# Kernel tuning notes

Hardware: AMD Instinct MI355X
Metric: run time of the kernel (lower is better)

The kernel has to match this reference:

```python
import jax, jax.numpy as jnp
import numpy as np

NR, K = 175, 250              # num_ranges, top_k
N = NR * K                    # 43750 active radar points
SHAPE0 = (56, 350, 512)       # (ele, range, azi) full-res sparse grid
SHAPE1 = (28, 175, 256)       # after stride-2 sparse conv
SHAPE2 = (14, 88, 128)        # after second stride-2 sparse conv
CAP1 = 350000                 # <= 8*N unique active cells after stride-2 conv
CAP2 = 69000                  # reachable region bound at stage 2 (14*88*56)
BC = 16                       # base_channel
C1, C2, CO = 2 * BC, 8 * BC, 128
OFFS = [(a, b, c) for a in range(3) for b in range(3) for c in range(3)]


def bn(x, p):
    # BatchNorm1d (eval form): p = [gamma, beta, running_mean, running_var]
    g, b, m, v = p
    return (x - m) * jax.lax.rsqrt(v + 1e-3) * g + b


def gn(x, groups, gamma, beta):
    n, c = x.shape
    xr = x.reshape(n, groups, c // groups)
    m = xr.mean(-1, keepdims=True)
    v = ((xr - m) ** 2).mean(-1, keepdims=True)
    return ((xr - m) * jax.lax.rsqrt(v + 1e-5)).reshape(n, c) * gamma + beta


def build_lut(coords, shape, n):
    # dense coord -> row-index map; out-of-bounds (padded) coords are dropped
    lut = jnp.full(shape, -1, jnp.int32)
    return lut.at[coords[:, 0], coords[:, 1], coords[:, 2]].set(jnp.arange(n, dtype=jnp.int32), mode='drop')


def subm_conv(feats, coords, lut, shape, w):
    # submanifold 3x3x3 conv: outputs only at active sites (gather-GEMM-accumulate)
    S = jnp.array(shape, jnp.int32)
    out = jnp.zeros((feats.shape[0], w.shape[-1]), feats.dtype)
    for k, off in enumerate(OFFS):
        nb = coords + (jnp.array(off, jnp.int32) - 1)
        inb = jnp.all((nb >= 0) & (nb < S), axis=-1)
        nbc = jnp.clip(nb, 0, S - 1)
        idx = lut[nbc[:, 0], nbc[:, 1], nbc[:, 2]]
        ok = inb & (idx >= 0)
        f = jnp.where(ok[:, None], feats[jnp.maximum(idx, 0)], 0.0)
        out = out + f @ w[k]
    return out


def down_conv(feats, coords_in, lut_in, shape_in, shape_out, cap, w):
    # SparseConv3d k=3 stride=2 pad=1: output sites = cells with any active input in receptive field
    mask = jnp.zeros(shape_in, bool).at[coords_in[:, 0], coords_in[:, 1], coords_in[:, 2]].set(True, mode='drop')
    pm = jnp.pad(mask, 1)
    om = jnp.zeros(shape_out, bool)
    for (a, b, c) in OFFS:
        om = om | pm[a:a + 2 * shape_out[0]:2, b:b + 2 * shape_out[1]:2, c:c + 2 * shape_out[2]:2]
    i0, i1, i2 = jnp.nonzero(om, size=cap, fill_value=0)
    oc = jnp.stack([i0, i1, i2], -1).astype(jnp.int32)
    valid = jnp.arange(cap) < om.sum()
    S = jnp.array(shape_in, jnp.int32)
    out = jnp.zeros((cap, w.shape[-1]), feats.dtype)
    for k, off in enumerate(OFFS):
        nb = 2 * oc + (jnp.array(off, jnp.int32) - 1)   # input coord = 2j + k - 1
        inb = jnp.all((nb >= 0) & (nb < S), axis=-1)
        nbc = jnp.clip(nb, 0, S - 1)
        idx = lut_in[nbc[:, 0], nbc[:, 1], nbc[:, 2]]
        ok = inb & (idx >= 0)
        f = jnp.where(ok[:, None], feats[jnp.maximum(idx, 0)], 0.0)
        out = out + f @ w[k]
    # padded (invalid) rows get out-of-bounds coords so later scatters/luts drop them
    oc_safe = jnp.where(valid[:, None], oc, jnp.array(shape_out, jnp.int32))
    return out, oc_safe


def basic_block(f, coords, lut, shape, w2, p2):
    h = jax.nn.relu(bn(subm_conv(f, coords, lut, shape, w2[0]), p2[0]))
    h = bn(subm_conv(h, coords, lut, shape, w2[1]), p2[1])
    return jax.nn.relu(h + f)


def range_attn(pw, c1, c3, ele_table, azi_table, wq, bq, wk, bk, wv, bv):
    x = pw.reshape(NR, K, 1)
    e = ele_table[c1.reshape(NR, K)]   # [NR,K,3]
    a = azi_table[c3.reshape(NR, K)]   # [NR,K,3]
    scale = 32.0 ** -0.5               # queries.size(-1) = hidden_dim = 32
    for l in range(4):
        xin = jnp.concatenate([x, e, a], -1)           # [NR,K,7]
        q = xin @ wq[l] + bq[l]
        kk = xin @ wk[l] + bk[l]
        v = xin @ wv[l] + bv[l]
        att = jax.nn.softmax(jnp.einsum('rkd,rjd->rkj', q, kk) * scale, axis=-1)
        x = jnp.einsum('rkj,rjd->rkd', att, v)         # [NR,K,1]
    return x.reshape(N, 1)


def forward(voxel_features, coors, ele_table, azi_table, wq, bq, wk, bk, wv, bv,
            w_in, b_in, gin_g, gin_b, w_d1, bn_d1, w_r1, bn_r1,
            w_d2, bn_d2, w_r2, bn_r2, w_out, b_out, gout_g, gout_b):
    c1, c2, c3 = coors[:, 1], coors[:, 2], coors[:, 3]
    pw = jnp.log10(voxel_features[:, -2])[:, None]
    f_att = range_attn(pw, c1, c3, ele_table, azi_table, wq, bq, wk, bk, wv, bv)
    ele = c1 * 2 - 9          # (56 - 37*2)//2 = -9
    rng = c2 * 2
    azi = c3 * 2 + 149        # (512 - 107*2)//2 = 149
    feats = jnp.concatenate([ele[:, None].astype(jnp.float32), rng[:, None].astype(jnp.float32),
                             azi[:, None].astype(jnp.float32), f_att], -1)   # [N,4]
    coords0 = jnp.stack([ele, rng, azi], -1).astype(jnp.int32)
    # conv_input: 1x1x1 SubMConv (per-point linear) + GroupNorm(8) + ReLU
    f0 = jax.nn.relu(gn(feats @ w_in + b_in, 8, gin_g, gin_b))
    lut0 = build_lut(coords0, SHAPE0, N)
    f1, oc1 = down_conv(f0, coords0, lut0, SHAPE0, SHAPE1, CAP1, w_d1)
    f1 = jax.nn.relu(bn(f1, bn_d1))
    lut1 = build_lut(oc1, SHAPE1, CAP1)
    f1 = basic_block(f1, oc1, lut1, SHAPE1, w_r1[0], bn_r1[0])
    f1 = basic_block(f1, oc1, lut1, SHAPE1, w_r1[1], bn_r1[1])
    f2, oc2 = down_conv(f1, oc1, lut1, SHAPE1, SHAPE2, CAP2, w_d2)
    f2 = jax.nn.relu(bn(f2, bn_d2))
    lut2 = build_lut(oc2, SHAPE2, CAP2)
    f2 = basic_block(f2, oc2, lut2, SHAPE2, w_r2[0], bn_r2[0])
    f2 = basic_block(f2, oc2, lut2, SHAPE2, w_r2[1], bn_r2[1])
    # conv_out: SubMConv3d(k=3, bias) + GroupNorm(16) + ReLU
    fo = subm_conv(f2, oc2, lut2, SHAPE2, w_out) + b_out
    fo = jax.nn.relu(gn(fo, 16, gout_g, gout_b))
    dense = jnp.zeros(SHAPE2 + (CO,), fo.dtype).at[oc2[:, 0], oc2[:, 1], oc2[:, 2]].set(fo, mode='drop')
    # torch dense: [1,C,ele,range,azi].permute(0,1,4,3,2) -> [1,C,azi,range,ele]
    return jnp.transpose(dense, (3, 2, 1, 0))[None]


def setup_inputs():
    key = jax.random.key(0)
    ks = iter(jax.random.split(key, 64))
    nrm = lambda shp, s: jax.random.normal(next(ks), shp, jnp.float32) * s

    def bnp(c):
        return jnp.stack([1.0 + nrm((c,), 0.1), nrm((c,), 0.1), nrm((c,), 0.05),
                          1.0 + 0.1 * jax.random.uniform(next(ks), (c,), jnp.float32)])

    voxel_features = jax.random.uniform(next(ks), (N, 2), jnp.float32, 0.1, 100.0)
    c0 = jnp.zeros((N,), jnp.int32)
    c1 = jax.random.randint(next(ks), (N,), 5, 33, jnp.int32)      # ele bin -> ele_ind in [1,55]
    c2 = jnp.repeat(jnp.arange(NR, dtype=jnp.int32), K)            # 250 points per range bin
    c3 = jax.random.randint(next(ks), (N,), 0, 107, jnp.int32)
    coors = jnp.stack([c0, c1, c2, c3], -1)
    return dict(
        voxel_features=voxel_features, coors=coors, batch_size=1,
        ele_table=nrm((37, 3), 1.0), azi_table=nrm((107, 3), 1.0),
        wq=nrm((4, 7, 32), 0.3), bq=nrm((4, 32), 0.1),
        wk=nrm((4, 7, 32), 0.3), bk=nrm((4, 32), 0.1),
        wv=nrm((4, 7, 1), 0.3), bv=nrm((4, 1), 0.1),
        w_in=nrm((4, BC), 0.5), b_in=nrm((BC,), 0.1),
        gin_g=1.0 + nrm((BC,), 0.1), gin_b=nrm((BC,), 0.1),
        w_d1=nrm((27, BC, C1), (27 * BC) ** -0.5), bn_d1=bnp(C1),
        w_r1=nrm((2, 2, 27, C1, C1), (27 * C1) ** -0.5),
        bn_r1=jnp.stack([jnp.stack([bnp(C1), bnp(C1)]), jnp.stack([bnp(C1), bnp(C1)])]),
        w_d2=nrm((27, C1, C2), (27 * C1) ** -0.5), bn_d2=bnp(C2),
        w_r2=nrm((2, 2, 27, C2, C2), (27 * C2) ** -0.5),
        bn_r2=jnp.stack([jnp.stack([bnp(C2), bnp(C2)]), jnp.stack([bnp(C2), bnp(C2)])]),
        w_out=nrm((27, C2, CO), (27 * C2) ** -0.5), b_out=nrm((CO,), 0.1),
        gout_g=1.0 + nrm((CO,), 0.1), gout_b=nrm((CO,), 0.1),
    )


def reference(voxel_features, coors, batch_size, ele_table, azi_table, wq, bq, wk, bk, wv, bv,
              w_in, b_in, gin_g, gin_b, w_d1, bn_d1, w_r1, bn_r1,
              w_d2, bn_d2, w_r2, bn_r2, w_out, b_out, gout_g, gout_b):
    assert batch_size == 1
    return forward(voxel_features, coors, ele_table, azi_table, wq, bq, wk, bk, wv, bv,
                   w_in, b_in, gin_g, gin_b, w_d1, bn_d1, w_r1, bn_r1,
                   w_d2, bn_d2, w_r2, bn_r2, w_out, b_out, gout_g, gout_b)
```

## Files before the change

kernel.cpp:

```cpp
#include <hip/hip_runtime.h>
#include <math.h>

#define NRR 175
#define KK 250
#define NN (NRR*KK)

#define S0_0 56
#define S0_1 350
#define S0_2 512
#define S1_0 28
#define S1_1 175
#define S1_2 256
#define S2_0 14
#define S2_1 88
#define S2_2 128
#define CAP1 350000
#define CAP2 69000
#define C1 32
#define C2 128
#define FOP 69632

#define CELLS0 (S0_0*S0_1*S0_2)
#define CELLS1 (S1_0*S1_1*S1_2)
#define CELLS2 (S2_0*S2_1*S2_2)

#define ATT_SCALE 0.17677669529663687f

typedef __attribute__((ext_vector_type(8))) __bf16 bf16x8;
typedef __attribute__((ext_vector_type(16))) float f32x16;

__device__ __forceinline__ unsigned short f2b(float x) {
    unsigned int u = __builtin_bit_cast(unsigned int, x);
    unsigned int r = u + 0x7FFFu + ((u >> 16) & 1u);
    return (unsigned short)(r >> 16);
}
__device__ __forceinline__ float b2f(unsigned short h) {
    return __builtin_bit_cast(float, (unsigned int)h << 16);
}

__device__ __forceinline__ int block_incl_scan(int v, int* s) {
    int t = threadIdx.x;
    s[t] = v; __syncthreads();
    #pragma unroll
    for (int d = 1; d < 256; d <<= 1) {
        int x = (t >= d) ? s[t - d] : 0;
        __syncthreads();
        s[t] += x;
        __syncthreads();
    }
    return s[t];
}

__device__ __forceinline__ void cand(int p, int So, int* o, int& no) {
    no = 0;
    if ((p & 1) == 0) {
        int q = p >> 1; if (q < So) o[no++] = q;
    } else {
        int q = (p - 1) >> 1; if (q < So) o[no++] = q;
        q = (p + 1) >> 1;     if (q < So) o[no++] = q;
    }
}

__global__ __launch_bounds__(256) void k_init(const float* __restrict__ vf,
                                              const int* __restrict__ coors,
                                              float* __restrict__ x,
                                              int* __restrict__ lut0,
                                              int* __restrict__ om1) {
    int i = blockIdx.x * 256 + threadIdx.x;
    if (i >= NN) return;
    x[i] = log10f(vf[i * 2]);
    int c1 = coors[i * 4 + 1], c2 = coors[i * 4 + 2], c3 = coors[i * 4 + 3];
    int e = 2 * c1 - 9, rg = 2 * c2, az = 2 * c3 + 149;
    atomicMax(&lut0[(e * S0_1 + rg) * S0_2 + az], i);
    int A[2], B[2], C[2]; int na, nb, nc;
    cand(e, S1_0, A, na); cand(rg, S1_1, B, nb); cand(az, S1_2, C, nc);
    for (int ia = 0; ia < na; ia++)
        for (int ib = 0; ib < nb; ib++)
            for (int ic = 0; ic < nc; ic++)
                om1[(A[ia] * S1_1 + B[ib]) * S1_2 + C[ic]] = 1;
}

#define QS 40
__global__ __launch_bounds__(256, 1) void k_attn(float* __restrict__ x_io,
    const int* __restrict__ coors,
    const float* __restrict__ et, const float* __restrict__ at,
    const float* __restrict__ wq, const float* __restrict__ bq,
    const float* __restrict__ wk, const float* __restrict__ bk,
    const float* __restrict__ wv, const float* __restrict__ bv) {
    __shared__ float xin[KK * 7];
    __shared__ unsigned short ksh_h[256 * QS];
    __shared__ unsigned short ksh_l[256 * QS];
    __shared__ float vsh[256];
    const int r = blockIdx.x;
    const int t = threadIdx.x;
    const int w = t >> 6, ln = t & 63, l31 = ln & 31, lh = ln >> 5;

    for (int i = t; i < KK; i += 256) {
        int gi = r * KK + i;
        xin[i * 7 + 0] = x_io[gi];
        int c1 = coors[gi * 4 + 1], c3 = coors[gi * 4 + 3];
        xin[i * 7 + 1] = et[c1 * 3 + 0]; xin[i * 7 + 2] = et[c1 * 3 + 1]; xin[i * 7 + 3] = et[c1 * 3 + 2];
        xin[i * 7 + 4] = at[c3 * 3 + 0]; xin[i * 7 + 5] = at[c3 * 3 + 1]; xin[i * 7 + 6] = at[c3 * 3 + 2];
    }
    __syncthreads();

    union U8 { bf16x8 v; unsigned short u[8]; };

    for (int l = 0; l < 4; l++) {
        const float* wql = wq + l * 7 * 32; const float* bql = bq + l * 32;
        const float* wkl = wk + l * 7 * 32; const float* bkl = bk + l * 32;
        const float* wvl = wv + l * 7;      const float  bvl = bv[l];
        float qh_f[32], ql_f[32];
        if (t < KK) {
            float xi[7];
            #pragma unroll
            for (int ci = 0; ci < 7; ci++) xi[ci] = xin[t * 7 + ci];
            float av = bvl;
            #pragma unroll
            for (int ci = 0; ci < 7; ci++) av += xi[ci] * wvl[ci];
            vsh[t] = av;
            #pragma unroll
            for (int d = 0; d < 32; d++) {
                float aq = bql[d], ak = bkl[d];
                #pragma unroll
                for (int ci = 0; ci < 7; ci++) { aq += xi[ci] * wql[ci * 32 + d]; ak += xi[ci] * wkl[ci * 32 + d]; }
                aq *= ATT_SCALE;
                float h = b2f(f2b(aq));
                qh_f[d] = h; ql_f[d] = aq - h;
                unsigned short k16 = f2b(ak);
                ksh_h[t * QS + d] = k16;
                ksh_l[t * QS + d] = f2b(ak - b2f(k16));
            }
        } else {
            #pragma unroll
            for (int d = 0; d < 32; d++) {
                qh_f[d] = 0.f; ql_f[d] = 0.f;
                ksh_h[t * QS + d] = 0; ksh_l[t * QS + d] = 0;
            }
            vsh[t] = 0.f;
        }
        __syncthreads();

        U8 Bh[2][2], Bl[2][2];
        #pragma unroll
        for (int b = 0; b < 2; b++) {
            int src = b * 32 + l31;
            #pragma unroll
            for (int ks = 0; ks < 2; ks++) {
                #pragma unroll
                for (int j = 0; j < 8; j++) {
                    float h0 = __shfl(qh_f[ks * 16 + j],     src, 64);
                    float h1 = __shfl(qh_f[ks * 16 + 8 + j], src, 64);
                    float l0 = __shfl(ql_f[ks * 16 + j],     src, 64);
                    float l1 = __shfl(ql_f[ks * 16 + 8 + j], src, 64);
                    Bh[b][ks].u[j] = f2b(lh ? h1 : h0);
                    Bl[b][ks].u[j] = f2b(lh ? l1 : l0);
                }
            }
        }

        float m[2]  = {-1e30f, -1e30f};
        float den[2] = {0.f, 0.f};
        float num[2] = {0.f, 0.f};

        for (int mt = 0; mt < 8; mt++) {
            U8 Ah[2], Al[2];
            int krow = mt * 32 + l31;
            #pragma unroll
            for (int ks = 0; ks < 2; ks++) {
                Ah[ks].v = *(const bf16x8*)&ksh_h[krow * QS + ks * 16 + lh * 8];
                Al[ks].v = *(const bf16x8*)&ksh_l[krow * QS + ks * 16 + lh * 8];
            }
            float4 v4[4];
            #pragma unroll
            for (int c = 0; c < 4; c++)
                v4[c] = *(const float4*)&vsh[mt * 32 + 8 * c + 4 * lh];

            #pragma unroll
            for (int b = 0; b < 2; b++) {
                f32x16 acc;
                #pragma unroll
                for (int q = 0; q < 16; q++) acc[q] = 0.f;
                acc = __builtin_amdgcn_mfma_f32_32x32x16_bf16(Ah[0].v, Bh[b][0].v, acc, 0, 0, 0);
                acc = __builtin_amdgcn_mfma_f32_32x32x16_bf16(Ah[1].v, Bh[b][1].v, acc, 0, 0, 0);
                acc = __builtin_amdgcn_mfma_f32_32x32x16_bf16(Ah[0].v, Bl[b][0].v, acc, 0, 0, 0);
                acc = __builtin_amdgcn_mfma_f32_32x32x16_bf16(Ah[1].v, Bl[b][1].v, acc, 0, 0, 0);
                acc = __builtin_amdgcn_mfma_f32_32x32x16_bf16(Al[0].v, Bh[b][0].v, acc, 0, 0, 0);
                acc = __builtin_amdgcn_mfma_f32_32x32x16_bf16(Al[1].v, Bh[b][1].v, acc, 0, 0, 0);

                float s[16];
                #pragma unroll
                for (int rr = 0; rr < 16; rr++) {
                    s[rr] = acc[rr];
                    if (mt == 7) {
                        int key = 224 + (rr & 3) + 8 * (rr >> 2) + 4 * lh;
                        if (key >= KK) s[rr] = -1e30f;
                    }
                }
                float cm = s[0];
                #pragma unroll
                for (int rr = 1; rr < 16; rr++) cm = fmaxf(cm, s[rr]);
                cm = fmaxf(cm, __shfl_xor(cm, 32, 64));
                float mn = fmaxf(m[b], cm);
                float alpha = __expf(m[b] - mn);
                float dsum = 0.f, nsum = 0.f;
                #pragma unroll
                for (int rr = 0; rr < 16; rr++) {
                    float e = __expf(s[rr] - mn);
                    dsum += e;
                    nsum += e * ((&v4[rr >> 2].x)[rr & 3]);
                }
                den[b] = den[b] * alpha + dsum;
                num[b] = num[b] * alpha + nsum;
                m[b] = mn;
            }
        }
        __syncthreads();
        #pragma unroll
        for (int b = 0; b < 2; b++) {
            float dtot = den[b] + __shfl_xor(den[b], 32, 64);
            float ntot = num[b] + __shfl_xor(num[b], 32, 64);
            int q = (w * 2 + b) * 32 + l31;
            if (lh == 0 && q < KK) xin[q * 7] = ntot / dtot;
        }
        __syncthreads();
    }
    for (int i = t; i < KK; i += 256) x_io[r * KK + i] = xin[i * 7];
}

__global__ __launch_bounds__(256) void k_f0(const int* __restrict__ coors,
    const float* __restrict__ x,
    const float* __restrict__ w_in, const float* __restrict__ b_in,
    const float* __restrict__ gg, const float* __restrict__ gb,
    unsigned short* __restrict__ f0) {
    int i = blockIdx.x * 256 + threadIdx.x;
    if (i >= NN) return;
    int c1 = coors[i * 4 + 1], c2 = coors[i * 4 + 2], c3 = coors[i * 4 + 3];
    float fe0 = (float)(2 * c1 - 9), fe1 = (float)(2 * c2), fe2 = (float)(2 * c3 + 149), fe3 = x[i];
    float tv[16];
    #pragma unroll
    for (int c = 0; c < 16; c++)
        tv[c] = b_in[c] + fe0 * w_in[c] + fe1 * w_in[16 + c] + fe2 * w_in[32 + c] + fe3 * w_in[48 + c];
    #pragma unroll
    for (int g = 0; g < 8; g++) {
        float a = tv[2 * g], b = tv[2 * g + 1];
        float m = 0.5f * (a + b);
        float va = 0.5f * ((a - m) * (a - m) + (b - m) * (b - m));
        float inv = rsqrtf(va + 1e-5f);
        f0[i * 16 + 2 * g]     = f2b(fmaxf((a - m) * inv * gg[2 * g]     + gb[2 * g],     0.f));
        f0[i * 16 + 2 * g + 1] = f2b(fmaxf((b - m) * inv * gg[2 * g + 1] + gb[2 * g + 1], 0.f));
    }
}

__global__ __launch_bounds__(256) void k_blocksum(const int* __restrict__ om,
                                                  int* __restrict__ partials, int ncells) {
    __shared__ int sh[256];
    int t = threadIdx.x;
    int base = blockIdx.x * 1024 + t * 4;
    int s = 0;
    #pragma unroll
    for (int q = 0; q < 4; q++) s += (base + q < ncells) ? om[base + q] : 0;
    int incl = block_incl_scan(s, sh);
    if (t == 255) partials[blockIdx.x] = incl;
}

__global__ __launch_bounds__(256) void k_scanparts(int* __restrict__ partials, int nparts,
                                                   int* __restrict__ pcnt, int cap) {
    __shared__ int sh[256];
    __shared__ int tot;
    int t = threadIdx.x;
    int chunk = (nparts + 255) / 256;
    int beg = t * chunk;
    int vals[8];
    int s = 0;
    #pragma unroll
    for (int i = 0; i < 8; i++) {
        if (i < chunk) {
            int ix = beg + i;
            int x = (ix < nparts) ? partials[ix] : 0;
            vals[i] = x; s += x;
        }
    }
    int incl = block_incl_scan(s, sh);
    int excl = incl - s;
    if (t == 255) tot = incl;
    int run = excl;
    #pragma unroll
    for (int i = 0; i < 8; i++) {
        if (i < chunk) {
            int ix = beg + i;
            if (ix < nparts) { partials[ix] = run; run += vals[i]; }
        }
    }
    __syncthreads();
    if (t == 0) *pcnt = min(tot, cap);
}

__global__ __launch_bounds__(256) void k_emit(const int* __restrict__ om,
                                              const int* __restrict__ partials,
                                              int* __restrict__ oc,
                                              int ncells, int D1, int D2, int cap) {
    __shared__ int sh[256];
    int t = threadIdx.x;
    int base = blockIdx.x * 1024 + t * 4;
    int v[4]; int s = 0;
    #pragma unroll
    for (int q = 0; q < 4; q++) { v[q] = (base + q < ncells) ? om[base + q] : 0; s += v[q]; }
    int incl = block_incl_scan(s, sh);
    int run = partials[blockIdx.x] + (incl - s);
    int D12 = D1 * D2;
    #pragma unroll
    for (int q = 0; q < 4; q++) {
        if (v[q]) {
            if (run < cap) {
                int lin = base + q;
                int i0 = lin / D12;
                int r2 = lin - i0 * D12;
                int i1 = r2 / D2;
                int i2 = r2 - i1 * D2;
                oc[run * 3] = i0; oc[run * 3 + 1] = i1; oc[run * 3 + 2] = i2;
            }
            run++;
        }
    }
}

__global__ __launch_bounds__(256) void k_lutscatter(const int* __restrict__ oc,
                                                    const int* __restrict__ pc,
                                                    int* __restrict__ lut, int D1, int D2) {
    int j = blockIdx.x * 256 + threadIdx.x;
    if (j >= *pc) return;
    lut[(oc[j * 3] * D1 + oc[j * 3 + 1]) * D2 + oc[j * 3 + 2]] = j;
}

__global__ __launch_bounds__(256) void k_mask2(const int* __restrict__ oc,
                                               const int* __restrict__ pc,
                                               int* __restrict__ om) {
    int j = blockIdx.x * 256 + threadIdx.x;
    if (j >= *pc) return;
    int p0 = oc[j * 3], p1 = oc[j * 3 + 1], p2 = oc[j * 3 + 2];
    int A[2], B[2], C[2]; int na, nb, nc;
    cand(p0, S2_0, A, na); cand(p1, S2_1, B, nb); cand(p2, S2_2, C, nc);
    for (int ia = 0; ia < na; ia++)
        for (int ib = 0; ib < nb; ib++)
            for (int ic = 0; ic < nc; ic++)
                om[(A[ia] * S2_1 + B[ib]) * S2_2 + C[ic]] = 1;
}

__global__ __launch_bounds__(256) void k_prepack(const float* __restrict__ w,
        unsigned short* __restrict__ wp, int nk, int cin, int cout) {
    int tid = blockIdx.x * 256 + threadIdx.x;
    int tot = nk * cin * cout;
    if (tid >= tot) return;
    int co = tid % cout; int rest = tid / cout; int ci = rest % cin; int kk = rest / cin;
    int ks = ci >> 4, kr = ci & 15, half = kr >> 3, j = kr & 7;
    int nt = co >> 5, cl = co & 31, lane = half * 32 + cl;
    wp[((((size_t)kk * (cin >> 4) + ks) * (cout >> 5) + nt) * 64 + lane) * 8 + j] = f2b(w[tid]);
}

template<int CIN, int COUT, int SD0, int SD1, int SD2, bool DOWN, int MODE>
__global__ __launch_bounds__(256)
void k_mconv(const unsigned short* __restrict__ fin, const int* __restrict__ lut,
             const int* __restrict__ oc, const int* __restrict__ pc,
             const unsigned short* __restrict__ wp,
             const float* __restrict__ p0, const float* __restrict__ p1,
             const float* __restrict__ p2,
             const unsigned short* __restrict__ res, void* __restrict__ fout_) {
    constexpr int KS = CIN / 16;
    constexpr int NT = COUT / 32;
    constexpr int SROW = CIN + 8;
    constexpr int CPR = CIN / 8;
    constexpr int HC  = CPR / 2;
    constexpr int TM  = (COUT == 128) ? 4 : 1;
    __shared__ unsigned short sA[128 * SROW];

    const int n = *pc;
    const int j0 = blockIdx.x * 128;
    if (j0 >= n) return;
    const int t = threadIdx.x;
    const int w = t >> 6, ln = t & 63, l31 = ln & 31, lh = ln >> 5;
    const int rowb = (COUT == 128) ? 0 : w * 32;
    const int colt = (COUT == 128) ? w : 0;

    const int srow = t >> 1;
    int cxs, cys, czs;
    {
        int j = j0 + srow;
        if (j < n) { cxs = oc[j * 3]; cys = oc[j * 3 + 1]; czs = oc[j * 3 + 2]; }
        else       { cxs = -1000000; cys = -1000000; czs = -1000000; }
    }
    const uint4* fin4 = (const uint4*)fin;

    auto lookup = [&](int kk) -> int {
        int dx = kk / 9 - 1, dy = (kk / 3) % 3 - 1, dz = kk % 3 - 1;
        int x, y, z;
        if (DOWN) { x = 2 * cxs + dx; y = 2 * cys + dy; z = 2 * czs + dz; }
        else      { x = cxs + dx; y = cys + dy; z = czs + dz; }
        if ((unsigned)x < (unsigned)SD0 && (unsigned)y < (unsigned)SD1 && (unsigned)z < (unsigned)SD2)
            return lut[(x * SD1 + y) * SD2 + z];
        return -1;
    };

    uint4 ld[HC];
    auto loadrow = [&](int idx) {
        #pragma unroll
        for (int q = 0; q < HC; q++) {
            uint4 v = make_uint4(0, 0, 0, 0);
            if (idx >= 0) v = fin4[(size_t)idx * CPR + (t & 1) * HC + q];
            ld[q] = v;
        }
    };

    f32x16 acc[TM];
    #pragma unroll
    for (int a = 0; a < TM; a++)
        #pragma unroll
        for (int q = 0; q < 16; q++) acc[a][q] = 0.f;

    int idxA = lookup(0);
    loadrow(idxA);
    int idxB = lookup(1);

    for (int k = 0; k < 27; k++) {
        __syncthreads();
        #pragma unroll
        for (int q = 0; q < HC; q++)
            *(uint4*)&sA[srow * SROW + ((t & 1) * HC + q) * 8] = ld[q];
        __syncthreads();
        if (k < 26) {
            loadrow(idxB);
            idxB = lookup(k + 2 <= 26 ? k + 2 : 26);
        }
        const unsigned short* wk = wp + (size_t)k * KS * NT * 512;
        #pragma unroll
        for (int ks = 0; ks < KS; ks++) {
            bf16x8 bfr = *(const bf16x8*)(wk + ((size_t)(ks * NT + colt) * 64 + ln) * 8);
            #pragma unroll
            for (int a = 0; a < TM; a++) {
                bf16x8 afr = *(const bf16x8*)(&sA[(rowb + a * 32 + l31) * SROW + ks * 16 + lh * 8]);
                acc[a] = __builtin_amdgcn_mfma_f32_32x32x16_bf16(afr, bfr, acc[a], 0, 0, 0);
            }
        }
    }

    const int co = colt * 32 + l31;
    if (MODE != 2) {
        unsigned short* fout = (unsigned short*)fout_;
        float g_ = p0[co], bb_ = p0[COUT + co], m_ = p0[2 * COUT + co];
        float iv = rsqrtf(p0[3 * COUT + co] + 1e-3f);
        #pragma unroll
        for (int a = 0; a < TM; a++) {
            #pragma unroll
            for (int r = 0; r < 16; r++) {
                int j = j0 + rowb + a * 32 + (r & 3) + 8 * (r >> 2) + 4 * lh;
                if (j < n) {
                    float y = (acc[a][r] - m_) * iv * g_ + bb_;
                    if (MODE == 1) y += b2f(res[(size_t)j * COUT + co]);
                    fout[(size_t)j * COUT + co] = f2b(fmaxf(y, 0.f));
                }
            }
        }
    } else {
        float* fo_t = (float*)fout_;
        float bias = p0[co], gg_ = p1[co], gb_ = p2[co];
        #pragma unroll
        for (int a = 0; a < TM; a++) {
            #pragma unroll
            for (int r = 0; r < 16; r++) {
                int j = j0 + a * 32 + (r & 3) + 8 * (r >> 2) + 4 * lh;
                float y = acc[a][r] + bias;
                float s = y;
                s += __shfl_xor(s, 1, 8);
                s += __shfl_xor(s, 2, 8);
                s += __shfl_xor(s, 4, 8);
                float m = s * 0.125f;
                float d = y - m;
                float q2 = d * d;
                q2 += __shfl_xor(q2, 1, 8);
                q2 += __shfl_xor(q2, 2, 8);
                q2 += __shfl_xor(q2, 4, 8);
                float var = q2 * 0.125f;
                float o = fmaxf(d * rsqrtf(var + 1e-5f) * gg_ + gb_, 0.f);
                fo_t[(size_t)co * FOP + j] = o;
            }
        }
    }
}

__global__ __launch_bounds__(256) void k_scatter(const float* __restrict__ fo_t,
                                                 const int* __restrict__ lut2,
                                                 float* __restrict__ dout) {
    int gid = blockIdx.x * 256 + threadIdx.x;
    int aa = gid % S2_0; int r = gid / S2_0;
    int bb = r % S2_1;   r /= S2_1;
    int cc = r % S2_2;   int co = r / S2_2;
    int idx = lut2[(aa * S2_1 + bb) * S2_2 + cc];
    float v = 0.f;
    if (idx >= 0) v = fo_t[(size_t)co * FOP + idx];
    dout[gid] = v;
}

extern "C" void kernel_launch(void* const* d_in, const int* in_sizes, int n_in,
                              void* d_out, int out_size, void* d_ws, size_t ws_size,
                              hipStream_t stream) {
    const float* vf    = (const float*)d_in[0];
    const int*   coors = (const int*)d_in[1];
    const float* et    = (const float*)d_in[3];
    const float* at    = (const float*)d_in[4];
    const float* wq    = (const float*)d_in[5];
    const float* bq    = (const float*)d_in[6];
    const float* wk_   = (const float*)d_in[7];
    const float* bk    = (const float*)d_in[8];
    const float* wv    = (const float*)d_in[9];
    const float* bv    = (const float*)d_in[10];
    const float* w_in  = (const float*)d_in[11];
    const float* b_in  = (const float*)d_in[12];
    const float* gin_g = (const float*)d_in[13];
    const float* gin_b = (const float*)d_in[14];
    const float* w_d1  = (const float*)d_in[15];
    const float* bn_d1 = (const float*)d_in[16];
    const float* w_r1  = (const float*)d_in[17];
    const float* bn_r1 = (const float*)d_in[18];
    const float* w_d2  = (const float*)d_in[19];
    const float* bn_d2 = (const float*)d_in[20];
    const float* w_r2  = (const float*)d_in[21];
    const float* bn_r2 = (const float*)d_in[22];
    const float* w_out = (const float*)d_in[23];
    const float* b_out = (const float*)d_in[24];
    const float* gout_g= (const float*)d_in[25];
    const float* gout_b= (const float*)d_in[26];

    char* ws = (char*)d_ws;
    size_t cur = 0;
    auto take = [&](size_t bytes) -> char* {
        char* p = ws + cur;
        cur += (bytes + 255) & ~(size_t)255;
        return p;
    };
    size_t usz1 = (size_t)4194304 + (size_t)CELLS0 * 4;
    size_t usz2 = (size_t)17694720 + (size_t)128 * FOP * 4;
    char* U = take(usz1 > usz2 ? usz1 : usz2);
    float*          x_att = (float*)U;
    unsigned short* f0    = (unsigned short*)(U + 262144);
    int*            lut0  = (int*)(U + 4194304);
    unsigned short* fB1   = (unsigned short*)U;
    unsigned short* fA2   = (unsigned short*)U;
    unsigned short* fB2   = (unsigned short*)(U + 17694720);
    float*          fo_t  = (float*)(U + 17694720);

    int*   om1      = (int*)take((size_t)CELLS1 * 4);
    int*   om2      = (int*)take((size_t)CELLS2 * 4);
    int*   partials = (int*)take(8192);
    int*   cnt      = (int*)take(256);
    int*   oc1      = (int*)take((size_t)CAP1 * 3 * 4);
    int*   oc2      = (int*)take((size_t)CAP2 * 3 * 4);
    unsigned short* fA1 = (unsigned short*)take((size_t)CAP1 * C1 * 2);
    int*   lut1     = (int*)take((size_t)CELLS1 * 4);
    int*   lut2     = (int*)take((size_t)CELLS2 * 4);
    unsigned short* wp_d1  = (unsigned short*)take((size_t)27 * 16 * 32 * 2);
    unsigned short* wp_r1  = (unsigned short*)take((size_t)108 * 32 * 32 * 2);
    unsigned short* wp_d2  = (unsigned short*)take((size_t)27 * 32 * 128 * 2);
    unsigned short* wp_r2  = (unsigned short*)take((size_t)108 * 128 * 128 * 2);
    unsigned short* wp_out = (unsigned short*)take((size_t)27 * 128 * 128 * 2);

    hipMemsetAsync(lut0, 0xFF, (size_t)CELLS0 * 4, stream);
    hipMemsetAsync(om1, 0, (size_t)CELLS1 * 4, stream);
    hipMemsetAsync(om2, 0, (size_t)CELLS2 * 4, stream);
    hipMemsetAsync(lut1, 0xFF, (size_t)CELLS1 * 4, stream);
    hipMemsetAsync(lut2, 0xFF, (size_t)CELLS2 * 4, stream);

    const int gN  = (NN + 255) / 256;
    const int gB1 = CELLS1 / 1024;
    const int gB2 = CELLS2 / 1024;
    const int gM1 = (CAP1 + 127) / 128;
    const int gM2 = (CAP2 + 127) / 128;
    const int gS1 = (CAP1 + 255) / 256;
    const int gS2 = (CAP2 + 255) / 256;

    k_prepack<<<(27*16*32   + 255)/256, 256, 0, stream>>>(w_d1,  wp_d1, 27, 16, 32);
    k_prepack<<<(108*32*32  + 255)/256, 256, 0, stream>>>(w_r1,  wp_r1, 108, 32, 32);
    k_prepack<<<(27*32*128  + 255)/256, 256, 0, stream>>>(w_d2,  wp_d2, 27, 32, 128);
    k_prepack<<<(108*128*128+ 255)/256, 256, 0, stream>>>(w_r2,  wp_r2, 108, 128, 128);
    k_prepack<<<(27*128*128 + 255)/256, 256, 0, stream>>>(w_out, wp_out, 27, 128, 128);

    k_init<<<gN, 256, 0, stream>>>(vf, coors, x_att, lut0, om1);
    k_attn<<<NRR, 256, 0, stream>>>(x_att, coors, et, at, wq, bq, wk_, bk, wv, bv);
    k_f0<<<gN, 256, 0, stream>>>(coors, x_att, w_in, b_in, gin_g, gin_b, f0);

    k_blocksum<<<gB1, 256, 0, stream>>>(om1, partials, CELLS1);
    k_scanparts<<<1, 256, 0, stream>>>(partials, gB1, cnt, CAP1);
    k_emit<<<gB1, 256, 0, stream>>>(om1, partials, oc1, CELLS1, S1_1, S1_2, CAP1);

    k_mconv<16, 32, S0_0, S0_1, S0_2, true, 0><<<gM1, 256, 0, stream>>>(
        f0, lut0, oc1, cnt, wp_d1, bn_d1, nullptr, nullptr, nullptr, fA1);
    k_lutscatter<<<gS1, 256, 0, stream>>>(oc1, cnt, lut1, S1_1, S1_2);

    k_mconv<32, 32, S1_0, S1_1, S1_2, false, 0><<<gM1, 256, 0, stream>>>(
        fA1, lut1, oc1, cnt, wp_r1 + 0 * 27648, bn_r1 + 0 * 128, nullptr, nullptr, nullptr, fB1);
    k_mconv<32, 32, S1_0, S1_1, S1_2, false, 1><<<gM1, 256, 0, stream>>>(
        fB1, lut1, oc1, cnt, wp_r1 + 1 * 27648, bn_r1 + 1 * 128, nullptr, nullptr, fA1, fA1);
    k_mconv<32, 32, S1_0, S1_1, S1_2, false, 0><<<gM1, 256, 0, stream>>>(
        fA1, lut1, oc1, cnt, wp_r1 + 2 * 27648, bn_r1 + 2 * 128, nullptr, nullptr, nullptr, fB1);
    k_mconv<32, 32, S1_0, S1_1, S1_2, false, 1><<<gM1, 256, 0, stream>>>(
        fB1, lut1, oc1, cnt, wp_r1 + 3 * 27648, bn_r1 + 3 * 128, nullptr, nullptr, fA1, fA1);

    k_mask2<<<gS1, 256, 0, stream>>>(oc1, cnt, om2);
    k_blocksum<<<gB2, 256, 0, stream>>>(om2, partials, CELLS2);
    k_scanparts<<<1, 256, 0, stream>>>(partials, gB2, cnt + 1, CAP2);
    k_emit<<<gB2, 256, 0, stream>>>(om2, partials, oc2, CELLS2, S2_1, S2_2, CAP2);

    k_mconv<32, 128, S1_0, S1_1, S1_2, true, 0><<<gM2, 256, 0, stream>>>(
        fA1, lut1, oc2, cnt + 1, wp_d2, bn_d2, nullptr, nullptr, nullptr, fA2);
    k_lutscatter<<<gS2, 256, 0, stream>>>(oc2, cnt + 1, lut2, S2_1, S2_2);

    const size_t wr2s = (size_t)27 * 128 * 128;
    k_mconv<128, 128, S2_0, S2_1, S2_2, false, 0><<<gM2, 256, 0, stream>>>(
        fA2, lut2, oc2, cnt + 1, wp_r2 + 0 * wr2s, bn_r2 + 0 * 512, nullptr, nullptr, nullptr, fB2);
    k_mconv<128, 128, S2_0, S2_1, S2_2, false, 1><<<gM2, 256, 0, stream>>>(
        fB2, lut2, oc2, cnt + 1, wp_r2 + 1 * wr2s, bn_r2 + 1 * 512, nullptr, nullptr, fA2, fA2);
    k_mconv<128, 128, S2_0, S2_1, S2_2, false, 0><<<gM2, 256, 0, stream>>>(
        fA2, lut2, oc2, cnt + 1, wp_r2 + 2 * wr2s, bn_r2 + 2 * 512, nullptr, nullptr, nullptr, fB2);
    k_mconv<128, 128, S2_0, S2_1, S2_2, false, 1><<<gM2, 256, 0, stream>>>(
        fB2, lut2, oc2, cnt + 1, wp_r2 + 3 * wr2s, bn_r2 + 3 * 512, nullptr, nullptr, fA2, fA2);

    k_mconv<128, 128, S2_0, S2_1, S2_2, false, 2><<<gM2, 256, 0, stream>>>(
        fA2, lut2, oc2, cnt + 1, wp_out, b_out, gout_g, gout_b, nullptr, fo_t);
    k_scatter<<<(S2_0 * S2_1 * S2_2 * 128) / 256, 256, 0, stream>>>(fo_t, lut2, (float*)d_out);
}
```

Baseline: 1.093 ms.

## Widen sparse conv blocks to 512 threads, swizzle XCDs, transpose scatter LUT

The sparse conv kernel is generalized to 512-thread blocks with a ROWS template parameter. Stage-1 blocks now cover 256 rows, and for 128-channel outputs the 8 waves split the work across row groups and column tiles. Block indices are remapped so consecutive row tiles land on the same XCD, and the B fragments for each k-slice are preloaded into registers before the MFMA loop. A transposed LUT is built for stage 2 so the final dense scatter reads the lookup table contiguously instead of with strided cell indexing. These changes trade extra register and LDS pressure per block for better reuse and memory locality.

```diff
diff --git a/kernel.cpp b/kernel.cpp
--- a/kernel.cpp
+++ b/kernel.cpp
@@ -36,6 +36,12 @@
 }
 __device__ __forceinline__ float b2f(unsigned short h) {
     return __builtin_bit_cast(float, (unsigned int)h << 16);
+}
+
+__device__ __forceinline__ int xcd_swizzle(int b, int nx) {
+    int per = nx >> 3, rem = nx & 7;
+    int x = b & 7, i = b >> 3;
+    return x * per + min(x, rem) + i;
 }
 
 __device__ __forceinline__ int block_incl_scan(int v, int* s) {
@@ -333,6 +339,17 @@
     lut[(oc[j * 3] * D1 + oc[j * 3 + 1]) * D2 + oc[j * 3 + 2]] = j;
 }
 
+__global__ __launch_bounds__(256) void k_lutscatter2(const int* __restrict__ oc,
+                                                     const int* __restrict__ pc,
+                                                     int* __restrict__ lut,
+                                                     int* __restrict__ lut_t) {
+    int j = blockIdx.x * 256 + threadIdx.x;
+    if (j >= *pc) return;
+    int a = oc[j * 3], b = oc[j * 3 + 1], c = oc[j * 3 + 2];
+    lut[(a * S2_1 + b) * S2_2 + c] = j;
+    lut_t[(c * S2_1 + b) * S2_0 + a] = j;
+}
+
 __global__ __launch_bounds__(256) void k_mask2(const int* __restrict__ oc,
                                                const int* __restrict__ pc,
                                                int* __restrict__ om) {
@@ -358,31 +375,34 @@
     wp[((((size_t)kk * (cin >> 4) + ks) * (cout >> 5) + nt) * 64 + lane) * 8 + j] = f2b(w[tid]);
 }
 
-template<int CIN, int COUT, int SD0, int SD1, int SD2, bool DOWN, int MODE>
-__global__ __launch_bounds__(256)
+template<int CIN, int COUT, int ROWS, int SD0, int SD1, int SD2, bool DOWN, int MODE>
+__global__ __launch_bounds__(512, 4)
 void k_mconv(const unsigned short* __restrict__ fin, const int* __restrict__ lut,
              const int* __restrict__ oc, const int* __restrict__ pc,
              const unsigned short* __restrict__ wp,
              const float* __restrict__ p0, const float* __restrict__ p1,
              const float* __restrict__ p2,
              const unsigned short* __restrict__ res, void* __restrict__ fout_) {
-    constexpr int KS = CIN / 16;
-    constexpr int NT = COUT / 32;
+    constexpr int KS   = CIN / 16;
+    constexpr int NT   = COUT / 32;
+    constexpr int RG   = 8 / NT;
+    constexpr int TM   = (ROWS / 32) / RG;
     constexpr int SROW = CIN + 8;
-    constexpr int CPR = CIN / 8;
-    constexpr int HC  = CPR / 2;
-    constexpr int TM  = (COUT == 128) ? 4 : 1;
-    __shared__ unsigned short sA[128 * SROW];
+    constexpr int CPR  = CIN / 8;
+    constexpr int HC   = (ROWS * CPR) / 512;
+    __shared__ unsigned short sA[ROWS * SROW];
 
     const int n = *pc;
-    const int j0 = blockIdx.x * 128;
+    const int blk = xcd_swizzle(blockIdx.x, gridDim.x);
+    const int j0 = blk * ROWS;
     if (j0 >= n) return;
     const int t = threadIdx.x;
     const int w = t >> 6, ln = t & 63, l31 = ln & 31, lh = ln >> 5;
-    const int rowb = (COUT == 128) ? 0 : w * 32;
-    const int colt = (COUT == 128) ? w : 0;
-
-    const int srow = t >> 1;
+    const int colt = w & (NT - 1);
+    const int rowb = (w / NT) * TM * 32;
+
+    const int srow = t & (ROWS - 1);
+    const int cb = (t / ROWS) * HC;
     int cxs, cys, czs;
     {
         int j = j0 + srow;
@@ -406,7 +426,7 @@
         #pragma unroll
         for (int q = 0; q < HC; q++) {
             uint4 v = make_uint4(0, 0, 0, 0);
-            if (idx >= 0) v = fin4[(size_t)idx * CPR + (t & 1) * HC + q];
+            if (idx >= 0) v = fin4[(size_t)idx * CPR + cb + q];
             ld[q] = v;
         }
     };
@@ -425,20 +445,23 @@
         __syncthreads();
         #pragma unroll
         for (int q = 0; q < HC; q++)
-            *(uint4*)&sA[srow * SROW + ((t & 1) * HC + q) * 8] = ld[q];
+            *(uint4*)&sA[srow * SROW + (cb + q) * 8] = ld[q];
         __syncthreads();
         if (k < 26) {
             loadrow(idxB);
             idxB = lookup(k + 2 <= 26 ? k + 2 : 26);
         }
         const unsigned short* wk = wp + (size_t)k * KS * NT * 512;
+        bf16x8 breg[KS];
+        #pragma unroll
+        for (int ks = 0; ks < KS; ks++)
+            breg[ks] = *(const bf16x8*)(wk + ((size_t)(ks * NT + colt) * 64 + ln) * 8);
         #pragma unroll
         for (int ks = 0; ks < KS; ks++) {
-            bf16x8 bfr = *(const bf16x8*)(wk + ((size_t)(ks * NT + colt) * 64 + ln) * 8);
             #pragma unroll
             for (int a = 0; a < TM; a++) {
                 bf16x8 afr = *(const bf16x8*)(&sA[(rowb + a * 32 + l31) * SROW + ks * 16 + lh * 8]);
-                acc[a] = __builtin_amdgcn_mfma_f32_32x32x16_bf16(afr, bfr, acc[a], 0, 0, 0);
+                acc[a] = __builtin_amdgcn_mfma_f32_32x32x16_bf16(afr, breg[ks], acc[a], 0, 0, 0);
             }
         }
     }
@@ -467,7 +490,7 @@
         for (int a = 0; a < TM; a++) {
             #pragma unroll
             for (int r = 0; r < 16; r++) {
-                int j = j0 + a * 32 + (r & 3) + 8 * (r >> 2) + 4 * lh;
+                int j = j0 + rowb + a * 32 + (r & 3) + 8 * (r >> 2) + 4 * lh;
                 float y = acc[a][r] + bias;
                 float s = y;
                 s += __shfl_xor(s, 1, 8);
@@ -488,13 +511,12 @@
 }
 
 __global__ __launch_bounds__(256) void k_scatter(const float* __restrict__ fo_t,
-                                                 const int* __restrict__ lut2,
+                                                 const int* __restrict__ lut2t,
                                                  float* __restrict__ dout) {
     int gid = blockIdx.x * 256 + threadIdx.x;
-    int aa = gid % S2_0; int r = gid / S2_0;
-    int bb = r % S2_1;   r /= S2_1;
-    int cc = r % S2_2;   int co = r / S2_2;
-    int idx = lut2[(aa * S2_1 + bb) * S2_2 + cc];
+    int cell = gid % CELLS2;
+    int co = gid / CELLS2;
+    int idx = lut2t[cell];
     float v = 0.f;
     if (idx >= 0) v = fo_t[(size_t)co * FOP + idx];
     dout[gid] = v;
@@ -557,6 +579,7 @@
     unsigned short* fA1 = (unsigned short*)take((size_t)CAP1 * C1 * 2);
     int*   lut1     = (int*)take((size_t)CELLS1 * 4);
     int*   lut2     = (int*)take((size_t)CELLS2 * 4);
+    int*   lut2t    = (int*)take((size_t)CELLS2 * 4);
     unsigned short* wp_d1  = (unsigned short*)take((size_t)27 * 16 * 32 * 2);
     unsigned short* wp_r1  = (unsigned short*)take((size_t)108 * 32 * 32 * 2);
     unsigned short* wp_d2  = (unsigned short*)take((size_t)27 * 32 * 128 * 2);
@@ -568,11 +591,12 @@
     hipMemsetAsync(om2, 0, (size_t)CELLS2 * 4, stream);
     hipMemsetAsync(lut1, 0xFF, (size_t)CELLS1 * 4, stream);
     hipMemsetAsync(lut2, 0xFF, (size_t)CELLS2 * 4, stream);
+    hipMemsetAsync(lut2t, 0xFF, (size_t)CELLS2 * 4, stream);
 
     const int gN  = (NN + 255) / 256;
     const int gB1 = CELLS1 / 1024;
     const int gB2 = CELLS2 / 1024;
-    const int gM1 = (CAP1 + 127) / 128;
+    const int gM1 = (CAP1 + 255) / 256;
     const int gM2 = (CAP2 + 127) / 128;
     const int gS1 = (CAP1 + 255) / 256;
     const int gS2 = (CAP2 + 255) / 256;
@@ -591,17 +615,17 @@
     k_scanparts<<<1, 256, 0, stream>>>(partials, gB1, cnt, CAP1);
     k_emit<<<gB1, 256, 0, stream>>>(om1, partials, oc1, CELLS1, S1_1, S1_2, CAP1);
 
-    k_mconv<16, 32, S0_0, S0_1, S0_2, true, 0><<<gM1, 256, 0, stream>>>(
+    k_mconv<16, 32, 256, S0_0, S0_1, S0_2, true, 0><<<gM1, 512, 0, stream>>>(
         f0, lut0, oc1, cnt, wp_d1, bn_d1, nullptr, nullptr, nullptr, fA1);
     k_lutscatter<<<gS1, 256, 0, stream>>>(oc1, cnt, lut1, S1_1, S1_2);
 
-    k_mconv<32, 32, S1_0, S1_1, S1_2, false, 0><<<gM1, 256, 0, stream>>>(
+    k_mconv<32, 32, 256, S1_0, S1_1, S1_2, false, 0><<<gM1, 512, 0, stream>>>(
         fA1, lut1, oc1, cnt, wp_r1 + 0 * 27648, bn_r1 + 0 * 128, nullptr, nullptr, nullptr, fB1);
-    k_mconv<32, 32, S1_0, S1_1, S1_2, false, 1><<<gM1, 256, 0, stream>>>(
+    k_mconv<32, 32, 256, S1_0, S1_1, S1_2, false, 1><<<gM1, 512, 0, stream>>>(
         fB1, lut1, oc1, cnt, wp_r1 + 1 * 27648, bn_r1 + 1 * 128, nullptr, nullptr, fA1, fA1);
-    k_mconv<32, 32, S1_0, S1_1, S1_2, false, 0><<<gM1, 256, 0, stream>>>(
+    k_mconv<32, 32, 256, S1_0, S1_1, S1_2, false, 0><<<gM1, 512, 0, stream>>>(
         fA1, lut1, oc1, cnt, wp_r1 + 2 * 27648, bn_r1 + 2 * 128, nullptr, nullptr, nullptr, fB1);
-    k_mconv<32, 32, S1_0, S1_1, S1_2, false, 1><<<gM1, 256, 0, stream>>>(
+    k_mconv<32, 32, 256, S1_0, S1_1, S1_2, false, 1><<<gM1, 512, 0, stream>>>(
         fB1, lut1, oc1, cnt, wp_r1 + 3 * 27648, bn_r1 + 3 * 128, nullptr, nullptr, fA1, fA1);
 
     k_mask2<<<gS1, 256, 0, stream>>>(oc1, cnt, om2);
@@ -609,21 +633,21 @@
     k_scanparts<<<1, 256, 0, stream>>>(partials, gB2, cnt + 1, CAP2);
     k_emit<<<gB2, 256, 0, stream>>>(om2, partials, oc2, CELLS2, S2_1, S2_2, CAP2);
 
-    k_mconv<32, 128, S1_0, S1_1, S1_2, true, 0><<<gM2, 256, 0, stream>>>(
+    k_mconv<32, 128, 128, S1_0, S1_1, S1_2, true, 0><<<gM2, 512, 0, stream>>>(
         fA1, lut1, oc2, cnt + 1, wp_d2, bn_d2, nullptr, nullptr, nullptr, fA2);
-    k_lutscatter<<<gS2, 256, 0, stream>>>(oc2, cnt + 1, lut2, S2_1, S2_2);
+    k_lutscatter2<<<gS2, 256, 0, stream>>>(oc2, cnt + 1, lut2, lut2t);
 
     const size_t wr2s = (size_t)27 * 128 * 128;
-    k_mconv<128, 128, S2_0, S2_1, S2_2, false, 0><<<gM2, 256, 0, stream>>>(
+    k_mconv<128, 128, 128, S2_0, S2_1, S2_2, false, 0><<<gM2, 512, 0, stream>>>(
         fA2, lut2, oc2, cnt + 1, wp_r2 + 0 * wr2s, bn_r2 + 0 * 512, nullptr, nullptr, nullptr, fB2);
-    k_mconv<128, 128, S2_0, S2_1, S2_2, false, 1><<<gM2, 256, 0, stream>>>(
+    k_mconv<128, 128, 128, S2_0, S2_1, S2_2, false, 1><<<gM2, 512, 0, stream>>>(
         fB2, lut2, oc2, cnt + 1, wp_r2 + 1 * wr2s, bn_r2 + 1 * 512, nullptr, nullptr, fA2, fA2);
-    k_mconv<128, 128, S2_0, S2_1, S2_2, false, 0><<<gM2, 256, 0, stream>>>(
+    k_mconv<128, 128, 128, S2_0, S2_1, S2_2, false, 0><<<gM2, 512, 0, stream>>>(
         fA2, lut2, oc2, cnt + 1, wp_r2 + 2 * wr2s, bn_r2 + 2 * 512, nullptr, nullptr, nullptr, fB2);
-    k_mconv<128, 128, S2_0, S2_1, S2_2, false, 1><<<gM2, 256, 0, stream>>>(
+    k_mconv<128, 128, 128, S2_0, S2_1, S2_2, false, 1><<<gM2, 512, 0, stream>>>(
         fB2, lut2, oc2, cnt + 1, wp_r2 + 3 * wr2s, bn_r2 + 3 * 512, nullptr, nullptr, fA2, fA2);
 
-    k_mconv<128, 128, S2_0, S2_1, S2_2, false, 2><<<gM2, 256, 0, stream>>>(
+    k_mconv<128, 128, 128, S2_0, S2_1, S2_2, false, 2><<<gM2, 512, 0, stream>>>(
         fA2, lut2, oc2, cnt + 1, wp_out, b_out, gout_g, gout_b, nullptr, fo_t);
-    k_scatter<<<(S2_0 * S2_1 * S2_2 * 128) / 256, 256, 0, stream>>>(fo_t, lut2, (float*)d_out);
-}
+    k_scatter<<<(S2_0 * S2_1 * S2_2 * 128) / 256, 256, 0, stream>>>(fo_t, lut2t, (float*)d_out);
+}
```

After: 1.426 ms. +30.4%, slower.
